# Optimization experiments

Hardware: AMD Instinct MI355X
Metric: run time of the kernel (lower is better)

The kernel has to match this reference:

```python
import jax, jax.numpy as jnp
from jax import lax
import numpy as np

L, B, D, H = 256, 128, 512, 512


def setup_inputs() -> dict:
    rng = np.random.default_rng(0)
    # random projective-ish dependency trees: node 0 is root, head[i] < i
    heads = np.full((B, L), -1, dtype=np.int64)
    for i in range(1, L):
        heads[:, i] = rng.integers(0, i, size=B)
    # bottom-up traversal order (children have larger index than parent)
    indexes = np.tile(np.arange(L - 1, -1, -1, dtype=np.int32)[:, None], (1, B))  # [L,B]
    # cm_full[b,p,j] = 1 if j is a child of p in tree b
    cm_full = (heads[:, None, :] == np.arange(L)[None, :, None]).astype(np.float32)  # [B,L,L]
    child_mask = cm_full[:, ::-1, :].transpose(1, 0, 2).copy()  # [L,B,L] aligned with indexes
    # top-down order: root first (ascending index works since head[i] < i)
    td_node = np.tile(np.arange(L, dtype=np.int32)[:, None], (1, B))  # [L,B]
    td_parent_idx = np.maximum(heads.T, 0).astype(np.int32)  # [L,B]
    td_parent_valid = (heads.T >= 0).astype(np.float32)  # [L,B], 0 at root
    root_index = np.zeros(B, dtype=np.int32)

    key = jax.random.key(0)
    ks = jax.random.split(key, 7)
    sx = 1.0 / np.sqrt(D)
    sh = 1.0 / np.sqrt(H)
    return {
        "emb": jax.random.normal(ks[0], (L, B, D), jnp.float32),
        "indexes": jnp.asarray(indexes),
        "child_mask": jnp.asarray(child_mask),
        "td_node": jnp.asarray(td_node),
        "td_parent_idx": jnp.asarray(td_parent_idx),
        "td_parent_valid": jnp.asarray(td_parent_valid),
        "root_index": jnp.asarray(root_index),
        "dt_Wx": jax.random.normal(ks[1], (D, 3 * H), jnp.float32) * sx,
        "dt_Uh": jax.random.normal(ks[2], (H, 3 * H), jnp.float32) * sh,
        "dt_b": jnp.zeros((3 * H,), jnp.float32),
        "td_Wx": jax.random.normal(ks[3], (D, 3 * H), jnp.float32) * sx,
        "td_Uh": jax.random.normal(ks[4], (H, 3 * H), jnp.float32) * sh,
        "td_b": jnp.zeros((3 * H,), jnp.float32),
    }


def _gru_cell(x, h, Wx, Uh, b):
    # standard GRU: gates laid out as [r, z, n]
    xg = x @ Wx + b
    hg = h @ Uh
    xr, xz, xn = jnp.split(xg, 3, axis=-1)
    hr, hz, hn = jnp.split(hg, 3, axis=-1)
    r = jax.nn.sigmoid(xr + hr)
    z = jax.nn.sigmoid(xz + hz)
    n = jnp.tanh(xn + r * hn)
    return (1.0 - z) * n + z * h


def reference(emb, indexes, child_mask, td_node, td_parent_idx, td_parent_valid,
              root_index, dt_Wx, dt_Uh, dt_b, td_Wx, td_Uh, td_b):
    Ld, Bd, Dd = emb.shape
    Hd = dt_Uh.shape[0]
    barange = jnp.arange(Bd)

    # ---- bottom-up (DT) pass: h_prev = sum of children hiddens ----
    x_dt = jnp.take_along_axis(emb, indexes[:, :, None], axis=0)  # [L,B,D]

    def dt_step(Hs, xs):
        x, node, cmask = xs                      # [B,D], [B], [B,L]
        h = jnp.einsum('bl,blh->bh', cmask, Hs)  # sum over children
        hn = _gru_cell(x, h, dt_Wx, dt_Uh, dt_b)
        return Hs.at[barange, node].set(hn), None

    Hdt, _ = lax.scan(dt_step, jnp.zeros((Bd, Ld, Hd), emb.dtype),
                      (x_dt, indexes, child_mask))

    # ---- top-down (TD) pass: h_prev = parent hidden (zeros at root) ----
    x_td = jnp.take_along_axis(emb, td_node[:, :, None], axis=0)  # [L,B,D]

    def td_step(Hs, xs):
        x, node, pidx, pvalid = xs
        h = Hs[barange, pidx] * pvalid[:, None]
        hn = _gru_cell(x, h, td_Wx, td_Uh, td_b)
        return Hs.at[barange, node].set(hn), None

    Htd, _ = lax.scan(td_step, jnp.zeros((Bd, Ld, Hd), emb.dtype),
                      (x_td, td_node, td_parent_idx, td_parent_valid))

    outputs = jnp.concatenate([Hdt, Htd], axis=-1)  # [B,L,2H] (batch-first as original)
    root_h = jnp.concatenate([Hdt[barange, root_index], Htd[barange, root_index]], axis=-1)
    output_t = root_h[None]  # [1,B,2H]
    return outputs, output_t
```

## Files before the change

kernel.cpp:

```cpp
#include <hip/hip_runtime.h>


#define NL 256
#define NB 128
#define NH 512
#define NG (NB * NL)

typedef short short8 __attribute__((ext_vector_type(8)));
typedef float f32x4 __attribute__((ext_vector_type(4)));

__device__ __forceinline__ float bf2f(unsigned short u) {
  union { unsigned int i; float f; } c; c.i = ((unsigned int)u) << 16; return c.f;
}
__device__ __forceinline__ unsigned short f2bf(float f) {
  union { float f; unsigned int i; } c; c.f = f;
  return (unsigned short)((c.i + 0x7FFFu + ((c.i >> 16) & 1u)) >> 16);
}
__device__ __forceinline__ short8 pk_bf16(f32x4 a, f32x4 b) {
  union { unsigned int u[4]; short8 s; } r;
  asm("v_cvt_pk_bf16_f32 %0, %1, %2" : "=v"(r.u[0]) : "v"(a[0]), "v"(a[1]));
  asm("v_cvt_pk_bf16_f32 %0, %1, %2" : "=v"(r.u[1]) : "v"(a[2]), "v"(a[3]));
  asm("v_cvt_pk_bf16_f32 %0, %1, %2" : "=v"(r.u[2]) : "v"(b[0]), "v"(b[1]));
  asm("v_cvt_pk_bf16_f32 %0, %1, %2" : "=v"(r.u[3]) : "v"(b[2]), "v"(b[3]));
  return r.s;
}
__device__ __forceinline__ void atom_pk_bf16(unsigned short* p, unsigned int ud) {
  asm volatile("global_atomic_pk_add_bf16 %0, %1, off" :: "v"((void*)p), "v"(ud) : "memory");
}
__device__ __forceinline__ void store_u32_wt(unsigned short* p, unsigned int v) {
  asm volatile("global_store_dword %0, %1, off sc0 sc1" :: "v"((void*)p), "v"(v) : "memory");
}

__device__ __forceinline__ void level_wait(unsigned int* c, unsigned int target) {
  if (threadIdx.x == 0) {
    while (__hip_atomic_load(c, __ATOMIC_RELAXED, __HIP_MEMORY_SCOPE_AGENT) < target)
      __builtin_amdgcn_s_sleep(2);
  }
  __syncthreads();
}

__global__ void prep_zero(f32x4* __restrict__ base, int n16) {
  const f32x4 z = {0.f, 0.f, 0.f, 0.f};
  int i = blockIdx.x * blockDim.x + threadIdx.x;
  int stride = gridDim.x * blockDim.x;
  for (int j = i; j < n16; j += stride) {
    asm volatile("global_store_dwordx4 %0, %1, off sc0 sc1 nt"
                 :: "v"((void*)(base + j)), "v"(z) : "memory");
  }
}

__global__ void prep_wt4(const float* __restrict__ w0, const float* __restrict__ w1,
                         const float* __restrict__ w2, const float* __restrict__ w3,
                         unsigned short* __restrict__ wt) {
  __shared__ float t[32][33];
  const float* w = blockIdx.z == 0 ? w0 : blockIdx.z == 1 ? w1 : blockIdx.z == 2 ? w2 : w3;
  unsigned short* dst = wt + (size_t)blockIdx.z * 1536 * 512;
  int n0 = blockIdx.x * 32, k0 = blockIdx.y * 32;
  int tx = threadIdx.x & 31, ty = threadIdx.x >> 5;
  #pragma unroll
  for (int i = 0; i < 4; ++i)
    t[ty + 8 * i][tx] = w[(size_t)(k0 + ty + 8 * i) * 1536 + n0 + tx];
  __syncthreads();
  #pragma unroll
  for (int i = 0; i < 4; ++i)
    dst[(size_t)(n0 + ty + 8 * i) * 512 + k0 + tx] = f2bf(t[tx][ty + 8 * i]);
}

__global__ void prep_sched(const int* __restrict__ td_pidx,
                           const float* __restrict__ td_pval,
                           int* __restrict__ sched, int* __restrict__ meta,
                           int* __restrict__ gidx, int* __restrict__ pslot) {
  __shared__ unsigned char dep[NB][NL];
  __shared__ unsigned short cnb[NB][256];
  __shared__ int cnt[256];
  __shared__ int off[257];
  __shared__ int dmax_s;
  const int tid = threadIdx.x;
  for (int j = tid; j < NB * 256; j += 256) ((unsigned short*)cnb)[j] = 0;
  if (tid == 0) dmax_s = 0;
  __syncthreads();
  if (tid < NB) {
    int b = tid, lmax = 0;
    for (int i = 0; i < NL; ++i) {
      float pv = td_pval[i * NB + b];
      int pi = td_pidx[i * NB + b];
      int d = (pv != 0.f) ? (int)dep[b][pi] + 1 : 0;
      dep[b][i] = (unsigned char)d;
      cnb[b][d]++;
      lmax = max(lmax, d);
    }
    atomicMax(&dmax_s, lmax);
  }
  __syncthreads();
  {
    int s = 0;
    for (int b = 0; b < NB; ++b) s += cnb[b][tid];
    cnt[tid] = s;
  }
  __syncthreads();
  if (tid == 0) {
    int s = 0;
    for (int d = 0; d < 256; ++d) { off[d] = s; s += cnt[d]; }
    off[256] = s;
  }
  __syncthreads();
  {
    int run = off[tid];
    for (int b = 0; b < NB; ++b) {
      int t = cnb[b][tid];
      cnb[b][tid] = (unsigned short)run;
      run += t;
    }
  }
  __syncthreads();
  if (tid < NB) {
    int b = tid;
    for (int i = 0; i < NL; ++i) {
      float pv = td_pval[i * NB + b];
      int pi = td_pidx[i * NB + b];
      int d = dep[b][i];
      int g = cnb[b][d]++;
      sched[g] = (b << 8) | i;
      gidx[b * NL + i] = g;
      pslot[g] = (pv != 0.f) ? gidx[b * NL + pi] : -1;
    }
  }
  if (tid == 0) meta[0] = dmax_s;
  __syncthreads();
  meta[1 + tid] = off[tid];
  meta[257 + tid] = cnt[tid];
}

__global__ void prep_xc(const float* __restrict__ emb, const int* __restrict__ sched,
                        unsigned short* __restrict__ Xc) {
  int g = blockIdx.x * 4 + (threadIdx.x >> 6);
  int lane = threadIdx.x & 63;
  int e = sched[g];
  int b = e >> 8, node = e & 255;
  const float* src = emb + ((size_t)node * NB + b) * 512 + lane * 8;
  f32x4 v0 = *(const f32x4*)src;
  f32x4 v1 = *(const f32x4*)(src + 4);
  *(short8*)(Xc + (size_t)g * 512 + lane * 8) = pk_bf16(v0, v1);
}

#define LDJ(j, rx, rh)                                            \
  { const int c_ = (ck + 1 + (j)) & 7;                            \
    rx[0] = *(const short8*)(sx + c_ * 64);                       \
    rx[1] = *(const short8*)(sx + c_ * 64 + 8);                   \
    rh[0] = *(const short8*)(sh + c_ * 64);                       \
    rh[1] = *(const short8*)(sh + c_ * 64 + 8); }
#define WRB(Xp, Hp, rx, rh)                                       \
  { *(short8*)((Xp) + srow * 128 + sw0) = rx[0];                  \
    *(short8*)((Xp) + srow * 128 + sw1) = rx[1];                  \
    *(short8*)((Hp) + srow * 128 + sw0) = rh[0];                  \
    *(short8*)((Hp) + srow * 128 + sw1) = rh[1]; }

__launch_bounds__(512, 2)
__global__ void tree_gru(const float* __restrict__ dt_b,
                         const float* __restrict__ td_b,
                         const unsigned short* __restrict__ wt,
                         const unsigned short* __restrict__ Xc,
                         unsigned short* __restrict__ Hdt,
                         unsigned short* __restrict__ Htd,
                         unsigned short* __restrict__ Hfd,
                         const unsigned short* __restrict__ zrow,
                         const int* __restrict__ meta,
                         const int* __restrict__ pslot,
                         unsigned int* __restrict__ ctr,
                         const int* __restrict__ sched,
                         const int* __restrict__ root_index,
                         float* __restrict__ out) {
  extern __shared__ unsigned char lds[];
  const int tid = threadIdx.x;
  const int bi  = blockIdx.x;
  const int cg   = bi >> 3;
  const int pass = (bi >> 2) & 1;
  const int rep  = bi & 3;
  const int w  = tid >> 6, l = tid & 63;
  const int lm = l & 15, kg = l >> 4;
  const int col = cg * 16 + lm;

  for (int idx = tid; idx < 6144; idx += 512) {
    int k8  = idx & 63;
    int n   = (idx >> 6) & 15;
    int g   = (idx >> 10) % 3;
    int mat = idx / 3072;
    const unsigned short* src = wt + (size_t)(pass * 2 + mat) * (1536 * 512)
                                   + (size_t)(g * 512 + cg * 16 + n) * 512 + k8 * 8;
    short8 v = *(const short8*)src;
    int off = ((mat * 3 + g) * 16 + n) * 1024 + ((k8 * 16) ^ ((n & 7) << 4));
    *(short8*)(lds + off) = v;
  }
  unsigned char* Xb0 = lds + 98304;
  unsigned char* Hb0 = Xb0 + 16384;
  unsigned char* Xb1 = Hb0 + 16384;
  unsigned char* Hb1 = Xb1 + 16384;
  __syncthreads();

  const float* bias = pass ? td_b : dt_b;
  const float br = bias[col], bz = bias[NH + col], bn = bias[2 * NH + col];
  const int base_wr = (0 * 16 + lm) * 1024;
  const int base_wz = (1 * 16 + lm) * 1024;
  const int base_wn = (2 * 16 + lm) * 1024;
  const int base_ur = (3 * 16 + lm) * 1024;
  const int base_uz = (4 * 16 + lm) * 1024;
  const int base_un = (5 * 16 + lm) * 1024;
  const int wswz = (lm & 7) << 4;
  const int srow = tid >> 2, sq = tid & 3;
  const int sw0 = ((sq * 2)     ^ (srow & 7)) << 4;
  const int sw1 = ((sq * 2 + 1) ^ (srow & 7)) << 4;
  const int ck = cg >> 2;
  const int ccw = 2 * ((cg & 3) * 16 + lm);
  const int ccslot = ccw >> 4, ccin = ccw & 15;
  const int Dmax = meta[0];
  unsigned int* doneP = ctr + pass * 256;

  for (int p = 0; p <= Dmax; ++p) {
    const int d = pass ? p : (Dmax - p);
    const int off_d = meta[1 + d];
    const int cnt_d = meta[257 + d];
    const int T = (cnt_d + 127) >> 7;
    if (T <= rep) continue;
    const int dl = pass ? d - 1 : d + 1;
    if (dl >= 0 && dl <= Dmax)
      level_wait(doneP + dl, (unsigned int)meta[257 + dl] * 32u);

    unsigned int myrows = 0;
    const unsigned short *sx, *sh;
    {
      const int gg = off_d + min(rep * 128 + srow, cnt_d - 1);
      sx = Xc + (size_t)gg * 512 + sq * 16;
      if (pass == 0) sh = Hdt + (size_t)gg * 512 + sq * 16;
      else { int ps = pslot[gg]; sh = (ps >= 0 ? Htd + (size_t)ps * 512 : zrow) + sq * 16; }
    }
    short8 x0[2], h0[2], x1[2], h1[2];
    LDJ(0, x0, h0);
    LDJ(1, x1, h1);

    for (int t = rep; t < T; t += 4) {
      const int g0 = off_d + t * 128;
      const int rows = min(128, cnt_d - t * 128);
      __syncthreads();
      WRB(Xb0, Hb0, x0, h0);
      LDJ(2, x0, h0);
      __syncthreads();

      f32x4 aR = {0,0,0,0}, aZ = {0,0,0,0}, aXN = {0,0,0,0}, aHN = {0,0,0,0};
      #pragma unroll
      for (int ci = 0; ci < 8; ++ci) {
        const int c = (ck + 1 + ci) & 7;
        const unsigned char* Ax = (ci & 1) ? Xb1 : Xb0;
        const unsigned char* Ah = (ci & 1) ? Hb1 : Hb0;
        #pragma unroll
        for (int ks = 0; ks < 2; ++ks) {
          const int so = (((ks << 2) | kg) ^ (lm & 7)) << 4;
          const int ar = (w * 16 + lm) * 128;
          short8 ax = *(const short8*)(Ax + ar + so);
          short8 ah = *(const short8*)(Ah + ar + so);
          const int kb = (c * 128 + ks * 64 + kg * 16) ^ wswz;
          short8 bwr = *(const short8*)(lds + base_wr + kb);
          short8 bwz = *(const short8*)(lds + base_wz + kb);
          short8 bwn = *(const short8*)(lds + base_wn + kb);
          short8 bur = *(const short8*)(lds + base_ur + kb);
          short8 buz = *(const short8*)(lds + base_uz + kb);
          short8 bun = *(const short8*)(lds + base_un + kb);
          aR  = __builtin_amdgcn_mfma_f32_16x16x32_bf16(ax, bwr, aR, 0, 0, 0);
          aZ  = __builtin_amdgcn_mfma_f32_16x16x32_bf16(ax, bwz, aZ, 0, 0, 0);
          aXN = __builtin_amdgcn_mfma_f32_16x16x32_bf16(ax, bwn, aXN, 0, 0, 0);
          aR  = __builtin_amdgcn_mfma_f32_16x16x32_bf16(ah, bur, aR, 0, 0, 0);
          aZ  = __builtin_amdgcn_mfma_f32_16x16x32_bf16(ah, buz, aZ, 0, 0, 0);
          aHN = __builtin_amdgcn_mfma_f32_16x16x32_bf16(ah, bun, aHN, 0, 0, 0);
        }
        if (ci < 7) {
          unsigned char* Wx = (ci & 1) ? Xb0 : Xb1;
          unsigned char* Wh = (ci & 1) ? Hb0 : Hb1;
          if ((ci & 1) == 0) {
            WRB(Wx, Wh, x1, h1);
            if (ci < 5) LDJ(ci + 3, x1, h1);
          } else {
            WRB(Wx, Wh, x0, h0);
            if (ci < 5) LDJ(ci + 3, x0, h0);
          }
          __syncthreads();
        }
      }
      float hv[4];
      #pragma unroll
      for (int q = 0; q < 4; ++q) {
        const int r = w * 16 + kg * 4 + q;
        const float hprev = bf2f(*(const unsigned short*)(
            Hb1 + r * 128 + (((ccslot ^ (r & 7)) << 4) | ccin)));
        float rr = 1.f / (1.f + __expf(-(aR[q] + br)));
        float zz = 1.f / (1.f + __expf(-(aZ[q] + bz)));
        float e2 = __expf(2.f * (aXN[q] + bn + rr * aHN[q]));
        float nn = (e2 - 1.f) / (e2 + 1.f);
        hv[q] = (1.f - zz) * nn + zz * hprev;
      }
      if (t + 4 < T) {
        const int gg = off_d + min((t + 4) * 128 + srow, cnt_d - 1);
        sx = Xc + (size_t)gg * 512 + sq * 16;
        if (pass == 0) sh = Hdt + (size_t)gg * 512 + sq * 16;
        else { int ps = pslot[gg]; sh = (ps >= 0 ? Htd + (size_t)ps * 512 : zrow) + sq * 16; }
        LDJ(0, x0, h0);
        LDJ(1, x1, h1);
      }
      #pragma unroll
      for (int q = 0; q < 4; ++q) {
        const int r = w * 16 + kg * 4 + q;
        if (r >= rows) continue;
        const int g = g0 + r;
        float ho = __shfl_xor(hv[q], 1);
        if (!(lm & 1)) {
          unsigned int ud;
          asm("v_cvt_pk_bf16_f32 %0, %1, %2" : "=v"(ud) : "v"(hv[q]), "v"(ho));
          if (pass == 0) {
            store_u32_wt(Hfd + (size_t)g * 512 + col, ud);
            int ps = pslot[g];
            if (ps >= 0) atom_pk_bf16(Hdt + (size_t)ps * 512 + col, ud);
          } else {
            store_u32_wt(Htd + (size_t)g * 512 + col, ud);
          }
        }
      }
      myrows += (unsigned int)rows;
    }
    asm volatile("s_waitcnt vmcnt(0)" ::: "memory");
    __syncthreads();
    if (tid == 0) {
      __hip_atomic_fetch_add(doneP + d, myrows,
                             __ATOMIC_RELAXED, __HIP_MEMORY_SCOPE_AGENT);
      __hip_atomic_fetch_add(ctr + 512 + pass, myrows,
                             __ATOMIC_RELAXED, __HIP_MEMORY_SCOPE_AGENT);
    }
  }

  level_wait(ctr + 512, (unsigned int)NG * 32u);
  level_wait(ctr + 513, (unsigned int)NG * 32u);
  #pragma unroll
  for (int it = 0; it < 4; ++it) {
    const int g = bi * 128 + it * 32 + (tid >> 4);
    const int part = tid & 15;
    const int e = sched[g];
    const int b = e >> 8, node = e & 255;
    float* dst = out + ((size_t)b * NL + node) * 1024;
    const bool isroot = (node == root_index[b]);
    float* dst2 = out + (size_t)NB * NL * 1024 + (size_t)b * 1024;
    const unsigned short* s1 = Hfd + (size_t)g * 512 + part * 32;
    const unsigned short* s2 = Htd + (size_t)g * 512 + part * 32;
    #pragma unroll
    for (int half = 0; half < 2; ++half) {
      const unsigned short* s = half ? s2 : s1;
      const int o = half * 512 + part * 32;
      #pragma unroll
      for (int j = 0; j < 4; ++j) {
        short8 v = *(const short8*)(s + j * 8);
        f32x4 lo, hi;
        #pragma unroll
        for (int q = 0; q < 4; ++q) {
          lo[q] = bf2f((unsigned short)v[q]);
          hi[q] = bf2f((unsigned short)v[4 + q]);
        }
        __builtin_nontemporal_store(lo, (f32x4*)(dst + o + j * 8));
        __builtin_nontemporal_store(hi, (f32x4*)(dst + o + j * 8 + 4));
        if (isroot) {
          *(f32x4*)(dst2 + o + j * 8) = lo;
          *(f32x4*)(dst2 + o + j * 8 + 4) = hi;
        }
      }
    }
  }
}

extern "C" void kernel_launch(void* const* d_in, const int* in_sizes, int n_in,
                              void* d_out, int out_size, void* d_ws, size_t ws_size,
                              hipStream_t stream) {
  (void)in_sizes; (void)n_in; (void)out_size; (void)ws_size;
  const float* emb      = (const float*)d_in[0];
  const int*   td_pidx  = (const int*)d_in[4];
  const float* td_pval  = (const float*)d_in[5];
  const int*   root_idx = (const int*)d_in[6];
  const float* dt_Wx    = (const float*)d_in[7];
  const float* dt_Uh    = (const float*)d_in[8];
  const float* dt_b     = (const float*)d_in[9];
  const float* td_Wx    = (const float*)d_in[10];
  const float* td_Uh    = (const float*)d_in[11];
  const float* td_b     = (const float*)d_in[12];
  float* out = (float*)d_out;

  unsigned short* wt   = (unsigned short*)d_ws;
  unsigned short* Xc   = wt + (size_t)4 * 1536 * 512;
  unsigned short* Hdt  = Xc + (size_t)NG * NH;
  unsigned short* Htd  = Hdt + (size_t)NG * NH;
  unsigned short* Hfd  = Htd + (size_t)NG * NH;
  unsigned short* zrow = Hfd + (size_t)NG * NH;
  unsigned int*   ctr  = (unsigned int*)(zrow + NH);
  int* sched = (int*)(ctr + 520);
  int* meta  = sched + NG;
  int* gidx  = meta + 520;
  int* pslot = gidx + NG;

  const int n16 = (int)(((size_t)3 * NG * NH * 2 + NH * 2 + 520 * 4) / 16);
  prep_zero<<<dim3(2048), dim3(256), 0, stream>>>((f32x4*)Hdt, n16);
  prep_wt4<<<dim3(48, 16, 4), dim3(256), 0, stream>>>(dt_Wx, dt_Uh, td_Wx, td_Uh, wt);
  prep_sched<<<dim3(1), dim3(256), 0, stream>>>(td_pidx, td_pval, sched, meta, gidx, pslot);
  prep_xc<<<dim3(NG / 4), dim3(256), 0, stream>>>(emb, sched, Xc);

  (void)hipFuncSetAttribute((const void*)tree_gru,
                            hipFuncAttributeMaxDynamicSharedMemorySize, 163840);

  void* args[] = {
    (void*)&dt_b, (void*)&td_b, (void*)&wt, (void*)&Xc, (void*)&Hdt, (void*)&Htd,
    (void*)&Hfd, (void*)&zrow, (void*)&meta, (void*)&pslot, (void*)&ctr,
    (void*)&sched, (void*)&root_idx, (void*)&out
  };
  (void)hipLaunchCooperativeKernel((const void*)tree_gru, dim3(256), dim3(512),
                                   args, 163840u, stream);
}
```

Before: 1.398 ms.

## Keep GRU weights in registers and split waves into x/h roles

Weight tiles now live in 48 short8 registers per lane rather than LDS, with half the waves computing the x-projection and half the h-projection. The x-projection partials go through a small LDS exchange buffer to the h waves, which apply the gates. Row tiles per block shrink from 128 to 64, which halves per-wave A-operand LDS traffic and removes the B-operand LDS reads. It costs heavy register pressure (192 VGPRs of weights under launch_bounds 512,2), which risks spills, and adds an extra barrier and LDS round trip per tile.

```diff
diff --git a/kernel.cpp b/kernel.cpp
--- a/kernel.cpp
+++ b/kernel.cpp
@@ -143,17 +143,13 @@
   *(short8*)(Xc + (size_t)g * 512 + lane * 8) = pk_bf16(v0, v1);
 }
 
-#define LDJ(j, rx, rh)                                            \
-  { const int c_ = (ck + 1 + (j)) & 7;                            \
-    rx[0] = *(const short8*)(sx + c_ * 64);                       \
-    rx[1] = *(const short8*)(sx + c_ * 64 + 8);                   \
-    rh[0] = *(const short8*)(sh + c_ * 64);                       \
-    rh[1] = *(const short8*)(sh + c_ * 64 + 8); }
-#define WRB(Xp, Hp, rx, rh)                                       \
-  { *(short8*)((Xp) + srow * 128 + sw0) = rx[0];                  \
-    *(short8*)((Xp) + srow * 128 + sw1) = rx[1];                  \
-    *(short8*)((Hp) + srow * 128 + sw0) = rh[0];                  \
-    *(short8*)((Hp) + srow * 128 + sw1) = rh[1]; }
+#define LDJ2(j, s)                                                 \
+  { const int c_ = (ck + 1 + (j)) & 7;                             \
+    s[0] = *(const short8*)(sp + c_ * 64);                         \
+    s[1] = *(const short8*)(sp + c_ * 64 + 8); }
+#define WRB2(buf, s)                                               \
+  { *(short8*)((buf) + srow * 128 + sw0) = s[0];                   \
+    *(short8*)((buf) + srow * 128 + sw1) = s[1]; }
 
 __launch_bounds__(512, 2)
 __global__ void tree_gru(const float* __restrict__ dt_b,
@@ -171,45 +167,49 @@
                          const int* __restrict__ root_index,
                          float* __restrict__ out) {
   extern __shared__ unsigned char lds[];
+  unsigned char* Xb0 = lds;
+  unsigned char* Xb1 = lds + 8192;
+  unsigned char* Hb0 = lds + 16384;
+  unsigned char* Hb1 = lds + 24576;
+  float* XACC = (float*)(lds + 32768);
+
   const int tid = threadIdx.x;
   const int bi  = blockIdx.x;
   const int cg   = bi >> 3;
   const int pass = (bi >> 2) & 1;
   const int rep  = bi & 3;
   const int w  = tid >> 6, l = tid & 63;
+  const int role = w & 1;
+  const int rg   = w >> 1;
   const int lm = l & 15, kg = l >> 4;
   const int col = cg * 16 + lm;
-
-  for (int idx = tid; idx < 6144; idx += 512) {
-    int k8  = idx & 63;
-    int n   = (idx >> 6) & 15;
-    int g   = (idx >> 10) % 3;
-    int mat = idx / 3072;
-    const unsigned short* src = wt + (size_t)(pass * 2 + mat) * (1536 * 512)
-                                   + (size_t)(g * 512 + cg * 16 + n) * 512 + k8 * 8;
-    short8 v = *(const short8*)src;
-    int off = ((mat * 3 + g) * 16 + n) * 1024 + ((k8 * 16) ^ ((n & 7) << 4));
-    *(short8*)(lds + off) = v;
-  }
-  unsigned char* Xb0 = lds + 98304;
-  unsigned char* Hb0 = Xb0 + 16384;
-  unsigned char* Xb1 = Hb0 + 16384;
-  unsigned char* Hb1 = Xb1 + 16384;
-  __syncthreads();
+  const int ck = cg >> 2;
+
+  const unsigned short* wtm = wt + (size_t)(pass * 2 + role) * (1536 * 512);
+  short8 B[48];
+  #pragma unroll
+  for (int ci = 0; ci < 8; ++ci) {
+    const int cc = (ck + 1 + ci) & 7;
+    #pragma unroll
+    for (int ks = 0; ks < 2; ++ks)
+      #pragma unroll
+      for (int g3 = 0; g3 < 3; ++g3)
+        B[(ci * 2 + ks) * 3 + g3] = *(const short8*)(
+            wtm + (size_t)(g3 * 512 + cg * 16 + lm) * 512 + cc * 64 + ks * 32 + kg * 8);
+  }
 
   const float* bias = pass ? td_b : dt_b;
   const float br = bias[col], bz = bias[NH + col], bn = bias[2 * NH + col];
-  const int base_wr = (0 * 16 + lm) * 1024;
-  const int base_wz = (1 * 16 + lm) * 1024;
-  const int base_wn = (2 * 16 + lm) * 1024;
-  const int base_ur = (3 * 16 + lm) * 1024;
-  const int base_uz = (4 * 16 + lm) * 1024;
-  const int base_un = (5 * 16 + lm) * 1024;
-  const int wswz = (lm & 7) << 4;
-  const int srow = tid >> 2, sq = tid & 3;
+  const int rtid = rg * 64 + l;
+  const int srow = rtid >> 2, sq = rtid & 3;
   const int sw0 = ((sq * 2)     ^ (srow & 7)) << 4;
   const int sw1 = ((sq * 2 + 1) ^ (srow & 7)) << 4;
-  const int ck = cg >> 2;
+  unsigned char* Sb0 = role ? Hb0 : Xb0;
+  unsigned char* Sb1 = role ? Hb1 : Xb1;
+  const unsigned char* Ar0 = role ? Hb0 : Xb0;
+  const unsigned char* Ar1 = role ? Hb1 : Xb1;
+  const int arow = (rg * 16 + lm) * 128;
+  const int rsw = (lm & 7) << 4;
   const int ccw = 2 * ((cg & 3) * 16 + lm);
   const int ccslot = ccw >> 4, ccin = ccw & 15;
   const int Dmax = meta[0];
@@ -219,106 +219,98 @@
     const int d = pass ? p : (Dmax - p);
     const int off_d = meta[1 + d];
     const int cnt_d = meta[257 + d];
-    const int T = (cnt_d + 127) >> 7;
+    const int T = (cnt_d + 63) >> 6;
     if (T <= rep) continue;
     const int dl = pass ? d - 1 : d + 1;
     if (dl >= 0 && dl <= Dmax)
       level_wait(doneP + dl, (unsigned int)meta[257 + dl] * 32u);
 
     unsigned int myrows = 0;
-    const unsigned short *sx, *sh;
+    const unsigned short* sp;
     {
-      const int gg = off_d + min(rep * 128 + srow, cnt_d - 1);
-      sx = Xc + (size_t)gg * 512 + sq * 16;
-      if (pass == 0) sh = Hdt + (size_t)gg * 512 + sq * 16;
-      else { int ps = pslot[gg]; sh = (ps >= 0 ? Htd + (size_t)ps * 512 : zrow) + sq * 16; }
-    }
-    short8 x0[2], h0[2], x1[2], h1[2];
-    LDJ(0, x0, h0);
-    LDJ(1, x1, h1);
+      const int gg = off_d + min(rep * 64 + srow, cnt_d - 1);
+      if (role == 0) sp = Xc + (size_t)gg * 512 + sq * 16;
+      else if (pass == 0) sp = Hdt + (size_t)gg * 512 + sq * 16;
+      else { int ps = pslot[gg]; sp = (ps >= 0 ? Htd + (size_t)ps * 512 : zrow) + sq * 16; }
+    }
+    short8 s0[2], s1[2];
+    LDJ2(0, s0);
+    LDJ2(1, s1);
 
     for (int t = rep; t < T; t += 4) {
-      const int g0 = off_d + t * 128;
-      const int rows = min(128, cnt_d - t * 128);
+      const int g0 = off_d + t * 64;
+      const int rows = min(64, cnt_d - t * 64);
       __syncthreads();
-      WRB(Xb0, Hb0, x0, h0);
-      LDJ(2, x0, h0);
+      WRB2(Sb0, s0);
+      LDJ2(2, s0);
       __syncthreads();
 
-      f32x4 aR = {0,0,0,0}, aZ = {0,0,0,0}, aXN = {0,0,0,0}, aHN = {0,0,0,0};
+      f32x4 a0 = {0,0,0,0}, a1 = {0,0,0,0}, a2 = {0,0,0,0};
       #pragma unroll
       for (int ci = 0; ci < 8; ++ci) {
-        const int c = (ck + 1 + ci) & 7;
-        const unsigned char* Ax = (ci & 1) ? Xb1 : Xb0;
-        const unsigned char* Ah = (ci & 1) ? Hb1 : Hb0;
+        const unsigned char* Ar = (ci & 1) ? Ar1 : Ar0;
         #pragma unroll
         for (int ks = 0; ks < 2; ++ks) {
           const int so = (((ks << 2) | kg) ^ (lm & 7)) << 4;
-          const int ar = (w * 16 + lm) * 128;
-          short8 ax = *(const short8*)(Ax + ar + so);
-          short8 ah = *(const short8*)(Ah + ar + so);
-          const int kb = (c * 128 + ks * 64 + kg * 16) ^ wswz;
-          short8 bwr = *(const short8*)(lds + base_wr + kb);
-          short8 bwz = *(const short8*)(lds + base_wz + kb);
-          short8 bwn = *(const short8*)(lds + base_wn + kb);
-          short8 bur = *(const short8*)(lds + base_ur + kb);
-          short8 buz = *(const short8*)(lds + base_uz + kb);
-          short8 bun = *(const short8*)(lds + base_un + kb);
-          aR  = __builtin_amdgcn_mfma_f32_16x16x32_bf16(ax, bwr, aR, 0, 0, 0);
-          aZ  = __builtin_amdgcn_mfma_f32_16x16x32_bf16(ax, bwz, aZ, 0, 0, 0);
-          aXN = __builtin_amdgcn_mfma_f32_16x16x32_bf16(ax, bwn, aXN, 0, 0, 0);
-          aR  = __builtin_amdgcn_mfma_f32_16x16x32_bf16(ah, bur, aR, 0, 0, 0);
-          aZ  = __builtin_amdgcn_mfma_f32_16x16x32_bf16(ah, buz, aZ, 0, 0, 0);
-          aHN = __builtin_amdgcn_mfma_f32_16x16x32_bf16(ah, bun, aHN, 0, 0, 0);
+          short8 a = *(const short8*)(Ar + arow + so);
+          a0 = __builtin_amdgcn_mfma_f32_16x16x32_bf16(a, B[(ci * 2 + ks) * 3 + 0], a0, 0, 0, 0);
+          a1 = __builtin_amdgcn_mfma_f32_16x16x32_bf16(a, B[(ci * 2 + ks) * 3 + 1], a1, 0, 0, 0);
+          a2 = __builtin_amdgcn_mfma_f32_16x16x32_bf16(a, B[(ci * 2 + ks) * 3 + 2], a2, 0, 0, 0);
         }
         if (ci < 7) {
-          unsigned char* Wx = (ci & 1) ? Xb0 : Xb1;
-          unsigned char* Wh = (ci & 1) ? Hb0 : Hb1;
-          if ((ci & 1) == 0) {
-            WRB(Wx, Wh, x1, h1);
-            if (ci < 5) LDJ(ci + 3, x1, h1);
-          } else {
-            WRB(Wx, Wh, x0, h0);
-            if (ci < 5) LDJ(ci + 3, x0, h0);
-          }
+          unsigned char* Wb = (ci & 1) ? Sb0 : Sb1;
+          if ((ci & 1) == 0) { WRB2(Wb, s1); if (ci < 5) LDJ2(ci + 3, s1); }
+          else               { WRB2(Wb, s0); if (ci < 5) LDJ2(ci + 3, s0); }
           __syncthreads();
         }
       }
+      if (role == 0) {
+        float* pb = XACC + (size_t)(rg * 64 + l) * 12;
+        *(f32x4*)(pb + 0) = a0; *(f32x4*)(pb + 4) = a1; *(f32x4*)(pb + 8) = a2;
+      }
+      __syncthreads();
       float hv[4];
-      #pragma unroll
-      for (int q = 0; q < 4; ++q) {
-        const int r = w * 16 + kg * 4 + q;
-        const float hprev = bf2f(*(const unsigned short*)(
-            Hb1 + r * 128 + (((ccslot ^ (r & 7)) << 4) | ccin)));
-        float rr = 1.f / (1.f + __expf(-(aR[q] + br)));
-        float zz = 1.f / (1.f + __expf(-(aZ[q] + bz)));
-        float e2 = __expf(2.f * (aXN[q] + bn + rr * aHN[q]));
-        float nn = (e2 - 1.f) / (e2 + 1.f);
-        hv[q] = (1.f - zz) * nn + zz * hprev;
+      if (role == 1) {
+        const float* pb = XACC + (size_t)(rg * 64 + l) * 12;
+        f32x4 xR = *(const f32x4*)(pb + 0);
+        f32x4 xZ = *(const f32x4*)(pb + 4);
+        f32x4 xN = *(const f32x4*)(pb + 8);
+        #pragma unroll
+        for (int q = 0; q < 4; ++q) {
+          const int r = rg * 16 + kg * 4 + q;
+          const float hprev = bf2f(*(const unsigned short*)(
+              Hb1 + r * 128 + (((ccslot ^ (r & 7)) << 4) | ccin)));
+          float rr = 1.f / (1.f + __expf(-(xR[q] + br + a0[q])));
+          float zz = 1.f / (1.f + __expf(-(xZ[q] + bz + a1[q])));
+          float e2 = __expf(2.f * (xN[q] + bn + rr * a2[q]));
+          float nn = (e2 - 1.f) / (e2 + 1.f);
+          hv[q] = (1.f - zz) * nn + zz * hprev;
+        }
       }
       if (t + 4 < T) {
-        const int gg = off_d + min((t + 4) * 128 + srow, cnt_d - 1);
-        sx = Xc + (size_t)gg * 512 + sq * 16;
-        if (pass == 0) sh = Hdt + (size_t)gg * 512 + sq * 16;
-        else { int ps = pslot[gg]; sh = (ps >= 0 ? Htd + (size_t)ps * 512 : zrow) + sq * 16; }
-        LDJ(0, x0, h0);
-        LDJ(1, x1, h1);
-      }
-      #pragma unroll
-      for (int q = 0; q < 4; ++q) {
-        const int r = w * 16 + kg * 4 + q;
-        if (r >= rows) continue;
-        const int g = g0 + r;
-        float ho = __shfl_xor(hv[q], 1);
-        if (!(lm & 1)) {
-          unsigned int ud;
-          asm("v_cvt_pk_bf16_f32 %0, %1, %2" : "=v"(ud) : "v"(hv[q]), "v"(ho));
-          if (pass == 0) {
-            store_u32_wt(Hfd + (size_t)g * 512 + col, ud);
-            int ps = pslot[g];
-            if (ps >= 0) atom_pk_bf16(Hdt + (size_t)ps * 512 + col, ud);
-          } else {
-            store_u32_wt(Htd + (size_t)g * 512 + col, ud);
+        const int gg = off_d + min((t + 4) * 64 + srow, cnt_d - 1);
+        if (role == 0) sp = Xc + (size_t)gg * 512 + sq * 16;
+        else if (pass == 0) sp = Hdt + (size_t)gg * 512 + sq * 16;
+        else { int ps = pslot[gg]; sp = (ps >= 0 ? Htd + (size_t)ps * 512 : zrow) + sq * 16; }
+        LDJ2(0, s0);
+        LDJ2(1, s1);
+      }
+      if (role == 1) {
+        #pragma unroll
+        for (int q = 0; q < 4; ++q) {
+          const int r = rg * 16 + kg * 4 + q;
+          float ho = __shfl_xor(hv[q], 1);
+          if (r < rows && !(lm & 1)) {
+            const int g = g0 + r;
+            unsigned int ud;
+            asm("v_cvt_pk_bf16_f32 %0, %1, %2" : "=v"(ud) : "v"(hv[q]), "v"(ho));
+            if (pass == 0) {
+              store_u32_wt(Hfd + (size_t)g * 512 + col, ud);
+              int ps = pslot[g];
+              if (ps >= 0) atom_pk_bf16(Hdt + (size_t)ps * 512 + col, ud);
+            } else {
+              store_u32_wt(Htd + (size_t)g * 512 + col, ud);
+            }
           }
         }
       }
@@ -345,11 +337,11 @@
     float* dst = out + ((size_t)b * NL + node) * 1024;
     const bool isroot = (node == root_index[b]);
     float* dst2 = out + (size_t)NB * NL * 1024 + (size_t)b * 1024;
-    const unsigned short* s1 = Hfd + (size_t)g * 512 + part * 32;
-    const unsigned short* s2 = Htd + (size_t)g * 512 + part * 32;
+    const unsigned short* sA = Hfd + (size_t)g * 512 + part * 32;
+    const unsigned short* sB = Htd + (size_t)g * 512 + part * 32;
     #pragma unroll
     for (int half = 0; half < 2; ++half) {
-      const unsigned short* s = half ? s2 : s1;
+      const unsigned short* s = half ? sB : sA;
       const int o = half * 512 + part * 32;
       #pragma unroll
       for (int j = 0; j < 4; ++j) {
@@ -406,7 +398,7 @@
   prep_xc<<<dim3(NG / 4), dim3(256), 0, stream>>>(emb, sched, Xc);
 
   (void)hipFuncSetAttribute((const void*)tree_gru,
-                            hipFuncAttributeMaxDynamicSharedMemorySize, 163840);
+                            hipFuncAttributeMaxDynamicSharedMemorySize, 45056);
 
   void* args[] = {
     (void*)&dt_b, (void*)&td_b, (void*)&wt, (void*)&Xc, (void*)&Hdt, (void*)&Htd,
@@ -414,5 +406,5 @@
     (void*)&sched, (void*)&root_idx, (void*)&out
   };
   (void)hipLaunchCooperativeKernel((const void*)tree_gru, dim3(256), dim3(512),
-                                   args, 163840u, stream);
-}
+                                   args, 45056u, stream);
+}
```

New measurement: 1.647 ms. 1.18x slower.
